# Kernel tuning notes

Hardware: AMD Instinct MI355X
Metric: run time of the kernel (lower is better)

The kernel has to match this reference:

```python
import jax, jax.numpy as jnp
import numpy as np

N_USER = 250_000
N_ITEM = 250_000
E = 500_000
IN, H, C = 128, 64, 2
NEG_SLOPE = 0.01  # torch F.leaky_relu default


def setup_inputs() -> dict:
    key = jax.random.key(0)
    ks = jax.random.split(key, 24)
    d = {}
    d["feat_user"] = jax.random.normal(ks[0], (N_USER, IN), jnp.float32)
    d["feat_item"] = jax.random.normal(ks[1], (N_ITEM, IN), jnp.float32)
    # per-etype linear params, layer 1 (in_feats -> h_dim)
    s1 = 1.0 / np.sqrt(IN)
    d["W1_follows"] = jax.random.normal(ks[2], (IN, H), jnp.float32) * s1
    d["b1_follows"] = jax.random.normal(ks[3], (H,), jnp.float32) * s1
    d["W1_clicks"]  = jax.random.normal(ks[4], (IN, H), jnp.float32) * s1
    d["b1_clicks"]  = jax.random.normal(ks[5], (H,), jnp.float32) * s1
    d["W1_rev"]     = jax.random.normal(ks[6], (IN, H), jnp.float32) * s1
    d["b1_rev"]     = jax.random.normal(ks[7], (H,), jnp.float32) * s1
    # per-etype linear params, layer 2 (h_dim -> num_classes)
    s2 = 1.0 / np.sqrt(H)
    d["W2_follows"] = jax.random.normal(ks[8], (H, C), jnp.float32) * s2
    d["b2_follows"] = jax.random.normal(ks[9], (C,), jnp.float32) * s2
    d["W2_clicks"]  = jax.random.normal(ks[10], (H, C), jnp.float32) * s2
    d["b2_clicks"]  = jax.random.normal(ks[11], (C,), jnp.float32) * s2
    d["W2_rev"]     = jax.random.normal(ks[12], (H, C), jnp.float32) * s2
    d["b2_rev"]     = jax.random.normal(ks[13], (C,), jnp.float32) * s2
    # edge lists: (src, dst) per canonical etype
    d["follows_src"] = jax.random.randint(ks[14], (E,), 0, N_USER, jnp.int32)  # user->user
    d["follows_dst"] = jax.random.randint(ks[15], (E,), 0, N_USER, jnp.int32)
    d["clicks_src"]  = jax.random.randint(ks[16], (E,), 0, N_USER, jnp.int32)  # user->item
    d["clicks_dst"]  = jax.random.randint(ks[17], (E,), 0, N_ITEM, jnp.int32)
    d["rev_src"]     = jax.random.randint(ks[18], (E,), 0, N_ITEM, jnp.int32)  # item->user
    d["rev_dst"]     = jax.random.randint(ks[19], (E,), 0, N_USER, jnp.int32)
    return d


def _mean_agg(Wh, src, dst, n_dst):
    # copy_u + mean: gather transformed src feats per edge, segment-mean onto dst
    m = Wh[src]                                                   # [E, d]
    s = jax.ops.segment_sum(m, dst, num_segments=n_dst)           # [n_dst, d]
    deg = jax.ops.segment_sum(jnp.ones_like(dst, Wh.dtype), dst, num_segments=n_dst)
    return s / jnp.maximum(deg, 1.0)[:, None]                     # 0 for deg-0 nodes (DGL fills 0)


def _layer(fu, fi, Wf, bf, Wc, bc, Wr, br,
           fsrc, fdst, csrc, cdst, rsrc, rdst):
    # per-etype linear on src features, per-etype mean, cross-etype 'sum'
    h_user = (_mean_agg(fu @ Wf + bf, fsrc, fdst, N_USER)
              + _mean_agg(fi @ Wr + br, rsrc, rdst, N_USER))
    h_item = _mean_agg(fu @ Wc + bc, csrc, cdst, N_ITEM)
    return h_user, h_item


def reference(feat_user, feat_item,
              W1_follows, b1_follows, W1_clicks, b1_clicks, W1_rev, b1_rev,
              W2_follows, b2_follows, W2_clicks, b2_clicks, W2_rev, b2_rev,
              follows_src, follows_dst, clicks_src, clicks_dst, rev_src, rev_dst):
    h1u, h1i = _layer(feat_user, feat_item,
                      W1_follows, b1_follows, W1_clicks, b1_clicks, W1_rev, b1_rev,
                      follows_src, follows_dst, clicks_src, clicks_dst, rev_src, rev_dst)
    h2u = jnp.where(h1u >= 0, h1u, NEG_SLOPE * h1u)
    h2i = jnp.where(h1i >= 0, h1i, NEG_SLOPE * h1i)
    out_u, out_i = _layer(h2u, h2i,
                          W2_follows, b2_follows, W2_clicks, b2_clicks, W2_rev, b2_rev,
                          follows_src, follows_dst, clicks_src, clicks_dst, rev_src, rev_dst)
    # (h_dict, h_dict_2) flattened per ntype
    return (out_u, out_i, h2u, h2i)
```

## Files before the change

kernel.cpp:

```cpp
#include <hip/hip_runtime.h>
#include <cstdio>

#define NU 250000
#define NI 250000
#define NE 500000
#define ND 250000
#define NB_SCAN 245
#define NR 8
#define RSZ 31250

typedef __attribute__((ext_vector_type(8))) short short8v;
typedef __attribute__((ext_vector_type(4))) float float4v;

__device__ inline unsigned short f2bf(float x) {
  unsigned int b = __float_as_uint(x);
  unsigned int r = (b + 0x7FFFu + ((b >> 16) & 1u)) >> 16;
  return (unsigned short)r;
}
__device__ inline float bf2f(unsigned short u) {
  return __uint_as_float(((unsigned int)u) << 16);
}

__device__ inline void async_copy16(const float* g, float* l) {
  __builtin_amdgcn_global_load_lds((const __attribute__((address_space(1))) void*)g,
                                   (__attribute__((address_space(3))) void*)l, 16, 0, 0);
}

__global__ void hist3_kernel(const int* __restrict__ fdst, const int* __restrict__ cdst,
                             const int* __restrict__ rdst,
                             int* __restrict__ degf, int* __restrict__ degc, int* __restrict__ degr) {
  int i = blockIdx.x * blockDim.x + threadIdx.x;
  if (i < NE) {
    atomicAdd(&degf[fdst[i]], 1);
    atomicAdd(&degc[cdst[i]], 1);
    atomicAdd(&degr[rdst[i]], 1);
  }
}

__global__ void scan1_kernel(const int* __restrict__ deg0, const int* __restrict__ deg1,
                             const int* __restrict__ deg2, int* __restrict__ bsum) {
  const int* deg = blockIdx.y == 0 ? deg0 : (blockIdx.y == 1 ? deg1 : deg2);
  int* bs = bsum + blockIdx.y * 256;
  __shared__ int s[256];
  int b = blockIdx.x, t = threadIdx.x;
  int base = b * 1024 + t * 4;
  int v = 0;
  #pragma unroll
  for (int i = 0; i < 4; ++i) if (base + i < ND) v += deg[base + i];
  s[t] = v; __syncthreads();
  for (int off = 128; off > 0; off >>= 1) { if (t < off) s[t] += s[t + off]; __syncthreads(); }
  if (t == 0) bs[b] = s[0];
}

__global__ void scan2_kernel(int* __restrict__ bsum) {
  int* bs = bsum + blockIdx.x * 256;
  __shared__ int s[256];
  int t = threadIdx.x;
  s[t] = (t < NB_SCAN) ? bs[t] : 0;
  __syncthreads();
  for (int off = 1; off < 256; off <<= 1) {
    int x = (t >= off) ? s[t - off] : 0;
    __syncthreads();
    s[t] += x;
    __syncthreads();
  }
  if (t < NB_SCAN) bs[t] = (t == 0) ? 0 : s[t - 1];
}

__global__ void scan3_kernel(const int* __restrict__ deg0, const int* __restrict__ deg1,
                             const int* __restrict__ deg2, const int* __restrict__ bsum,
                             int* __restrict__ offs0, int* __restrict__ offs1, int* __restrict__ offs2,
                             int* __restrict__ cur0, int* __restrict__ cur1, int* __restrict__ cur2) {
  int y = blockIdx.y;
  const int* deg = y == 0 ? deg0 : (y == 1 ? deg1 : deg2);
  int* offs = y == 0 ? offs0 : (y == 1 ? offs1 : offs2);
  int* cursor = y == 0 ? cur0 : (y == 1 ? cur1 : cur2);
  const int* bs = bsum + y * 256;
  __shared__ int s[256];
  int b = blockIdx.x, t = threadIdx.x;
  int base = b * 1024 + t * 4;
  int v[4]; int sum = 0;
  #pragma unroll
  for (int i = 0; i < 4; ++i) { v[i] = (base + i < ND) ? deg[base + i] : 0; sum += v[i]; }
  s[t] = sum; __syncthreads();
  for (int off = 1; off < 256; off <<= 1) {
    int x = (t >= off) ? s[t - off] : 0;
    __syncthreads();
    s[t] += x;
    __syncthreads();
  }
  int run = bs[b] + s[t] - sum;
  #pragma unroll
  for (int i = 0; i < 4; ++i) {
    if (base + i < ND) { offs[base + i] = run; cursor[base + i] = run; run += v[i]; }
  }
  if (b == 0 && t == 0) offs[ND] = NE;
}

__global__ void bucket_part_kernel(const int* __restrict__ fsrc, const int* __restrict__ fdst,
                                   const int* __restrict__ csrc, const int* __restrict__ cdst,
                                   const int* __restrict__ rsrc, const int* __restrict__ rdst,
                                   int* __restrict__ curf, int* __restrict__ curc, int* __restrict__ curr,
                                   int* __restrict__ srtf, int* __restrict__ srtc, int* __restrict__ srtr) {
  const int r = blockIdx.x & (NR - 1);
  const int chunk = blockIdx.x >> 3;
  const int lo = r * RSZ, hi = lo + RSZ;
  const int base = chunk * 1024;
  #pragma unroll
  for (int i = 0; i < 4; ++i) {
    int e = base + i * 256 + threadIdx.x;
    if (e < NE) {
      int d0 = fdst[e]; int s0 = fsrc[e];
      if (d0 >= lo && d0 < hi) { int p = atomicAdd(&curf[d0], 1); srtf[p] = s0; }
      int d1 = cdst[e]; int s1 = csrc[e];
      if (d1 >= lo && d1 < hi) { int p = atomicAdd(&curc[d1], 1); srtc[p] = s1; }
      int d2 = rdst[e]; int s2 = rsrc[e];
      if (d2 >= lo && d2 < hi) { int p = atomicAdd(&curr[d2], 1); srtr[p] = s2; }
    }
  }
}

__global__ void prepw_kernel(const float* __restrict__ W0, const float* __restrict__ W1,
                             const float* __restrict__ W2, unsigned short* __restrict__ T) {
  int gt = blockIdx.x * 256 + threadIdx.x;
  int et = gt >> 10;
  int g = gt & 1023;
  int gl = g & 63;
  int jm = (g >> 6) & 3;
  int c = g >> 8;
  int kb = c * 32 + (gl >> 4) * 8;
  int col = jm * 16 + (gl & 15);
  const float* W = et == 0 ? W0 : (et == 1 ? W1 : W2);
  short8v u;
  #pragma unroll
  for (int i = 0; i < 8; ++i) u[i] = (short)f2bf(W[(kb + i) * 64 + col]);
  ((short8v*)T)[gt] = u;
}

template <bool TWO>
__global__ __launch_bounds__(256, 2) void gemm_dma_kernel(
    const float* __restrict__ X, int n, int ntiles,
    const unsigned short* __restrict__ Ta, const float* __restrict__ ba,
    const unsigned short* __restrict__ Tb, const float* __restrict__ bb,
    unsigned short* __restrict__ Ya, unsigned short* __restrict__ Yb) {
  __shared__ float sx[2][64 * 128];
  const int tid = threadIdx.x;
  const int lane = tid & 63;
  const int wave = tid >> 6;
  const int cb = (lane >> 4) * 4;

  short8v A[4][4], B[4][4];
  #pragma unroll
  for (int c = 0; c < 4; ++c) {
    #pragma unroll
    for (int jm = 0; jm < 4; ++jm) {
      A[c][jm] = ((const short8v*)Ta)[c * 256 + jm * 64 + lane];
      if constexpr (TWO) B[c][jm] = ((const short8v*)Tb)[c * 256 + jm * 64 + lane];
    }
  }
  float4 bias_a[4], bias_b[4];
  #pragma unroll
  for (int jm = 0; jm < 4; ++jm) {
    bias_a[jm] = *(const float4*)&ba[jm * 16 + cb];
    if constexpr (TWO) bias_b[jm] = *(const float4*)&bb[jm * 16 + cb];
  }

  const int nl = wave * 16 + (lane & 15);
  const int sw = nl & 7;

  int t = blockIdx.x;
  {
    #pragma unroll
    for (int j = 0; j < 8; ++j) {
      int idx = (wave * 8 + j) * 64 + lane;
      int row = idx >> 5, u = idx & 31;
      int gr = t * 64 + row; if (gr >= n) gr = n - 1;
      const float* src = X + (size_t)gr * 128 + ((u ^ (row & 7)) << 2);
      float* dst = &sx[0][(wave * 8 + j) * 256];
      async_copy16(src, dst);
    }
  }
  asm volatile("s_waitcnt vmcnt(0)" ::: "memory");
  __syncthreads();

  int cur = 0;
  while (true) {
    int tn = t + (int)gridDim.x;
    bool more = (tn < ntiles);
    if (more) {
      #pragma unroll
      for (int j = 0; j < 8; ++j) {
        int idx = (wave * 8 + j) * 64 + lane;
        int row = idx >> 5, u = idx & 31;
        int gr = tn * 64 + row; if (gr >= n) gr = n - 1;
        const float* src = X + (size_t)gr * 128 + ((u ^ (row & 7)) << 2);
        float* dst = &sx[cur ^ 1][(wave * 8 + j) * 256];
        async_copy16(src, dst);
      }
    }

    float4v accA[4] = {};
    float4v accB[4] = {};
    #pragma unroll
    for (int c = 0; c < 4; ++c) {
      int s0 = c * 8 + (lane >> 4) * 2;
      float4 f0 = *(const float4*)&sx[cur][nl * 128 + (((s0 + 0) ^ sw) << 2)];
      float4 f1 = *(const float4*)&sx[cur][nl * 128 + (((s0 + 1) ^ sw) << 2)];
      short8v bfr;
      bfr[0] = (short)f2bf(f0.x); bfr[1] = (short)f2bf(f0.y);
      bfr[2] = (short)f2bf(f0.z); bfr[3] = (short)f2bf(f0.w);
      bfr[4] = (short)f2bf(f1.x); bfr[5] = (short)f2bf(f1.y);
      bfr[6] = (short)f2bf(f1.z); bfr[7] = (short)f2bf(f1.w);
      #pragma unroll
      for (int jm = 0; jm < 4; ++jm) {
        accA[jm] = __builtin_amdgcn_mfma_f32_16x16x32_bf16(A[c][jm], bfr, accA[jm], 0, 0, 0);
        if constexpr (TWO)
          accB[jm] = __builtin_amdgcn_mfma_f32_16x16x32_bf16(B[c][jm], bfr, accB[jm], 0, 0, 0);
      }
    }
    int node = t * 64 + nl;
    if (node < n) {
      #pragma unroll
      for (int jm = 0; jm < 4; ++jm) {
        ushort4 o;
        o.x = f2bf(accA[jm][0] + bias_a[jm].x);
        o.y = f2bf(accA[jm][1] + bias_a[jm].y);
        o.z = f2bf(accA[jm][2] + bias_a[jm].z);
        o.w = f2bf(accA[jm][3] + bias_a[jm].w);
        *(ushort4*)&Ya[(size_t)node * 64 + jm * 16 + cb] = o;
        if constexpr (TWO) {
          ushort4 o2;
          o2.x = f2bf(accB[jm][0] + bias_b[jm].x);
          o2.y = f2bf(accB[jm][1] + bias_b[jm].y);
          o2.z = f2bf(accB[jm][2] + bias_b[jm].z);
          o2.w = f2bf(accB[jm][3] + bias_b[jm].w);
          *(ushort4*)&Yb[(size_t)node * 64 + jm * 16 + cb] = o2;
        }
      }
    }

    if (!more) break;
    asm volatile("s_waitcnt vmcnt(0)" ::: "memory");
    __syncthreads();
    cur ^= 1;
    t = tn;
  }
}

__global__ __launch_bounds__(256) void agg_fused_kernel(
    const unsigned short* __restrict__ Whf, const unsigned short* __restrict__ Whr,
    const unsigned short* __restrict__ Whc,
    const int* __restrict__ offs_f, const int* __restrict__ srt_f,
    const int* __restrict__ offs_r, const int* __restrict__ srt_r,
    const int* __restrict__ offs_c, const int* __restrict__ srt_c,
    const float* __restrict__ W2f, const float* __restrict__ b2f,
    const float* __restrict__ W2c, const float* __restrict__ b2c,
    const float* __restrict__ W2r, const float* __restrict__ b2r,
    float* __restrict__ h2u, float* __restrict__ h2i,
    float* __restrict__ Y2f, float* __restrict__ Y2c, float* __restrict__ Y2r,
    int ub) {
  const int tid = threadIdx.x;
  const int gid = tid >> 4;
  const int q = tid & 15;

  if (blockIdx.x < ub) {
    int d0 = (blockIdx.x * 16 + gid) * 2;
    int d1 = d0 + 1;
    bool v0 = d0 < NU, v1 = d1 < NU;
    int ef0 = v0 ? offs_f[d0] : 0, ef0e = v0 ? offs_f[d0 + 1] : 0;
    int ef1 = v1 ? offs_f[d1] : 0, ef1e = v1 ? offs_f[d1 + 1] : 0;
    int er0 = v0 ? offs_r[d0] : 0, er0e = v0 ? offs_r[d0 + 1] : 0;
    int er1 = v1 ? offs_r[d1] : 0, er1e = v1 ? offs_r[d1 + 1] : 0;
    float rf0 = 1.0f / fmaxf((float)(ef0e - ef0), 1.0f);
    float rf1 = 1.0f / fmaxf((float)(ef1e - ef1), 1.0f);
    float rr0 = 1.0f / fmaxf((float)(er0e - er0), 1.0f);
    float rr1 = 1.0f / fmaxf((float)(er1e - er1), 1.0f);

    float af0[4] = {0, 0, 0, 0}, af1[4] = {0, 0, 0, 0};
    float ar0[4] = {0, 0, 0, 0}, ar1[4] = {0, 0, 0, 0};
    while (ef0 < ef0e || ef1 < ef1e || er0 < er0e || er1 < er1e) {
      bool hf0 = ef0 < ef0e, hf1 = ef1 < ef1e, hr0 = er0 < er0e, hr1 = er1 < er1e;
      ushort4 vf0, vf1, vr0, vr1;
      if (hf0) { int s = srt_f[ef0]; vf0 = *(const ushort4*)&Whf[(size_t)s * 64 + q * 4]; }
      if (hf1) { int s = srt_f[ef1]; vf1 = *(const ushort4*)&Whf[(size_t)s * 64 + q * 4]; }
      if (hr0) { int s = srt_r[er0]; vr0 = *(const ushort4*)&Whr[(size_t)s * 64 + q * 4]; }
      if (hr1) { int s = srt_r[er1]; vr1 = *(const ushort4*)&Whr[(size_t)s * 64 + q * 4]; }
      if (hf0) { af0[0] += bf2f(vf0.x); af0[1] += bf2f(vf0.y); af0[2] += bf2f(vf0.z); af0[3] += bf2f(vf0.w); ++ef0; }
      if (hf1) { af1[0] += bf2f(vf1.x); af1[1] += bf2f(vf1.y); af1[2] += bf2f(vf1.z); af1[3] += bf2f(vf1.w); ++ef1; }
      if (hr0) { ar0[0] += bf2f(vr0.x); ar0[1] += bf2f(vr0.y); ar0[2] += bf2f(vr0.z); ar0[3] += bf2f(vr0.w); ++er0; }
      if (hr1) { ar1[0] += bf2f(vr1.x); ar1[1] += bf2f(vr1.y); ar1[2] += bf2f(vr1.z); ar1[3] += bf2f(vr1.w); ++er1; }
    }

    float h0v[4], h1v[4];
    #pragma unroll
    for (int i = 0; i < 4; ++i) {
      float x0 = af0[i] * rf0 + ar0[i] * rr0;
      h0v[i] = x0 >= 0.f ? x0 : 0.01f * x0;
      float x1 = af1[i] * rf1 + ar1[i] * rr1;
      h1v[i] = x1 >= 0.f ? x1 : 0.01f * x1;
    }
    if (v0) *(float4*)&h2u[(size_t)d0 * 64 + q * 4] = make_float4(h0v[0], h0v[1], h0v[2], h0v[3]);
    if (v1) *(float4*)&h2u[(size_t)d1 * 64 + q * 4] = make_float4(h1v[0], h1v[1], h1v[2], h1v[3]);

    float pf00 = 0, pf01 = 0, pc00 = 0, pc01 = 0;
    float pf10 = 0, pf11 = 0, pc10 = 0, pc11 = 0;
    #pragma unroll
    for (int i = 0; i < 4; ++i) {
      int j = q * 4 + i;
      float wf0 = W2f[j * 2 + 0], wf1 = W2f[j * 2 + 1];
      float wc0 = W2c[j * 2 + 0], wc1 = W2c[j * 2 + 1];
      pf00 += h0v[i] * wf0; pf01 += h0v[i] * wf1;
      pc00 += h0v[i] * wc0; pc01 += h0v[i] * wc1;
      pf10 += h1v[i] * wf0; pf11 += h1v[i] * wf1;
      pc10 += h1v[i] * wc0; pc11 += h1v[i] * wc1;
    }
    #pragma unroll
    for (int off = 1; off < 16; off <<= 1) {
      pf00 += __shfl_xor(pf00, off, 64); pf01 += __shfl_xor(pf01, off, 64);
      pc00 += __shfl_xor(pc00, off, 64); pc01 += __shfl_xor(pc01, off, 64);
      pf10 += __shfl_xor(pf10, off, 64); pf11 += __shfl_xor(pf11, off, 64);
      pc10 += __shfl_xor(pc10, off, 64); pc11 += __shfl_xor(pc11, off, 64);
    }
    if (q == 0) {
      if (v0) {
        Y2f[(size_t)d0 * 2 + 0] = pf00 + b2f[0]; Y2f[(size_t)d0 * 2 + 1] = pf01 + b2f[1];
        Y2c[(size_t)d0 * 2 + 0] = pc00 + b2c[0]; Y2c[(size_t)d0 * 2 + 1] = pc01 + b2c[1];
      }
      if (v1) {
        Y2f[(size_t)d1 * 2 + 0] = pf10 + b2f[0]; Y2f[(size_t)d1 * 2 + 1] = pf11 + b2f[1];
        Y2c[(size_t)d1 * 2 + 0] = pc10 + b2c[0]; Y2c[(size_t)d1 * 2 + 1] = pc11 + b2c[1];
      }
    }
  } else {
    int d0 = ((blockIdx.x - ub) * 16 + gid) * 2;
    int d1 = d0 + 1;
    bool v0 = d0 < NI, v1 = d1 < NI;
    int ec0 = v0 ? offs_c[d0] : 0, ec0e = v0 ? offs_c[d0 + 1] : 0;
    int ec1 = v1 ? offs_c[d1] : 0, ec1e = v1 ? offs_c[d1 + 1] : 0;
    float rc0 = 1.0f / fmaxf((float)(ec0e - ec0), 1.0f);
    float rc1 = 1.0f / fmaxf((float)(ec1e - ec1), 1.0f);

    float ac0[4] = {0, 0, 0, 0}, ac1[4] = {0, 0, 0, 0};
    while (ec0 < ec0e || ec1 < ec1e) {
      bool h0 = ec0 < ec0e, h1 = ec1 < ec1e;
      ushort4 v0v, v1v;
      if (h0) { int s = srt_c[ec0]; v0v = *(const ushort4*)&Whc[(size_t)s * 64 + q * 4]; }
      if (h1) { int s = srt_c[ec1]; v1v = *(const ushort4*)&Whc[(size_t)s * 64 + q * 4]; }
      if (h0) { ac0[0] += bf2f(v0v.x); ac0[1] += bf2f(v0v.y); ac0[2] += bf2f(v0v.z); ac0[3] += bf2f(v0v.w); ++ec0; }
      if (h1) { ac1[0] += bf2f(v1v.x); ac1[1] += bf2f(v1v.y); ac1[2] += bf2f(v1v.z); ac1[3] += bf2f(v1v.w); ++ec1; }
    }

    float h0v[4], h1v[4];
    #pragma unroll
    for (int i = 0; i < 4; ++i) {
      float x0 = ac0[i] * rc0;
      h0v[i] = x0 >= 0.f ? x0 : 0.01f * x0;
      float x1 = ac1[i] * rc1;
      h1v[i] = x1 >= 0.f ? x1 : 0.01f * x1;
    }
    if (v0) *(float4*)&h2i[(size_t)d0 * 64 + q * 4] = make_float4(h0v[0], h0v[1], h0v[2], h0v[3]);
    if (v1) *(float4*)&h2i[(size_t)d1 * 64 + q * 4] = make_float4(h1v[0], h1v[1], h1v[2], h1v[3]);

    float p00 = 0, p01 = 0, p10 = 0, p11 = 0;
    #pragma unroll
    for (int i = 0; i < 4; ++i) {
      int j = q * 4 + i;
      float w0 = W2r[j * 2 + 0], w1 = W2r[j * 2 + 1];
      p00 += h0v[i] * w0; p01 += h0v[i] * w1;
      p10 += h1v[i] * w0; p11 += h1v[i] * w1;
    }
    #pragma unroll
    for (int off = 1; off < 16; off <<= 1) {
      p00 += __shfl_xor(p00, off, 64); p01 += __shfl_xor(p01, off, 64);
      p10 += __shfl_xor(p10, off, 64); p11 += __shfl_xor(p11, off, 64);
    }
    if (q == 0) {
      if (v0) { Y2r[(size_t)d0 * 2 + 0] = p00 + b2r[0]; Y2r[(size_t)d0 * 2 + 1] = p01 + b2r[1]; }
      if (v1) { Y2r[(size_t)d1 * 2 + 0] = p10 + b2r[0]; Y2r[(size_t)d1 * 2 + 1] = p11 + b2r[1]; }
    }
  }
}

__global__ void out_fused_kernel(const float* __restrict__ Y2f, const float* __restrict__ Y2r,
                                 const float* __restrict__ Y2c,
                                 const int* __restrict__ offs_f, const int* __restrict__ srt_f,
                                 const int* __restrict__ offs_r, const int* __restrict__ srt_r,
                                 const int* __restrict__ offs_c, const int* __restrict__ srt_c,
                                 float* __restrict__ out_u, float* __restrict__ out_i, int ub) {
  if (blockIdx.x < ub) {
    int d = blockIdx.x * 256 + threadIdx.x;
    if (d >= NU) return;
    int f = offs_f[d], f1 = offs_f[d + 1];
    int r = offs_r[d], r1 = offs_r[d + 1];
    float rf = 1.0f / fmaxf((float)(f1 - f), 1.0f);
    float rr = 1.0f / fmaxf((float)(r1 - r), 1.0f);
    float a0 = 0.f, a1 = 0.f, c0 = 0.f, c1 = 0.f;
    while (f < f1 || r < r1) {
      bool hf = f < f1, hr = r < r1;
      float2 yf, yr;
      if (hf) { int s = srt_f[f]; yf = *(const float2*)&Y2f[(size_t)s * 2]; }
      if (hr) { int s = srt_r[r]; yr = *(const float2*)&Y2r[(size_t)s * 2]; }
      if (hf) { a0 += yf.x; a1 += yf.y; ++f; }
      if (hr) { c0 += yr.x; c1 += yr.y; ++r; }
    }
    out_u[(size_t)d * 2 + 0] = a0 * rf + c0 * rr;
    out_u[(size_t)d * 2 + 1] = a1 * rf + c1 * rr;
  } else {
    int d = (blockIdx.x - ub) * 256 + threadIdx.x;
    if (d >= NI) return;
    int c = offs_c[d], c1e = offs_c[d + 1];
    float rc = 1.0f / fmaxf((float)(c1e - c), 1.0f);
    float a0 = 0.f, a1 = 0.f;
    for (; c < c1e; ++c) {
      int s = srt_c[c];
      a0 += Y2c[(size_t)s * 2 + 0]; a1 += Y2c[(size_t)s * 2 + 1];
    }
    out_i[(size_t)d * 2 + 0] = a0 * rc;
    out_i[(size_t)d * 2 + 1] = a1 * rc;
  }
}

extern "C" void kernel_launch(void* const* d_in, const int* in_sizes, int n_in,
                              void* d_out, int out_size, void* d_ws, size_t ws_size,
                              hipStream_t stream) {
  const float* feat_user = (const float*)d_in[0];
  const float* feat_item = (const float*)d_in[1];
  const float* W1f = (const float*)d_in[2];  const float* b1f = (const float*)d_in[3];
  const float* W1c = (const float*)d_in[4];  const float* b1c = (const float*)d_in[5];
  const float* W1r = (const float*)d_in[6];  const float* b1r = (const float*)d_in[7];
  const float* W2f = (const float*)d_in[8];  const float* b2f = (const float*)d_in[9];
  const float* W2c = (const float*)d_in[10]; const float* b2c = (const float*)d_in[11];
  const float* W2r = (const float*)d_in[12]; const float* b2r = (const float*)d_in[13];
  const int* fsrc = (const int*)d_in[14];  const int* fdst = (const int*)d_in[15];
  const int* csrc = (const int*)d_in[16];  const int* cdst = (const int*)d_in[17];
  const int* rsrc = (const int*)d_in[18];  const int* rdst = (const int*)d_in[19];

  float* out = (float*)d_out;
  float* out_u = out;
  float* out_i = out + 2 * NU;
  float* h2u  = out + 1000000;
  float* h2i  = out + 17000000;

  unsigned short* Whf = (unsigned short*)d_ws;
  unsigned short* Whc = Whf + 16000000;
  unsigned short* Whr = Whc + 16000000;
  unsigned short* Wtab = Whr + 16000000;
  unsigned short* Tf = Wtab;
  unsigned short* Tc = Wtab + 8192;
  unsigned short* Tr = Wtab + 16384;
  int* ibase = (int*)(Wtab + 24576);
  const int P = 250304;
  int* offs_f = ibase;            int* offs_c = offs_f + P;  int* offs_r = offs_c + P;
  int* cur_f  = offs_r + P;       int* cur_c  = cur_f + P;   int* cur_r  = cur_c + P;
  int* deg_f  = cur_r + P;        int* deg_c  = deg_f + P;   int* deg_r  = deg_c + P;
  int* srt_f  = deg_r + P;
  int* srt_c  = srt_f + 500096;
  int* srt_r  = srt_c + 500096;
  int* bsum   = srt_r + 500096;
  float* Y2f  = (float*)(bsum + 768);
  float* Y2c  = Y2f + 500000;
  float* Y2r  = Y2c + 500000;

  size_t need = 96000000ull + 24576ull * 2ull
              + (9ull * P + 3ull * 500096ull + 768ull + 1500000ull) * 4ull;
  if (ws_size < need) {
    fprintf(stderr, "kernel_launch: ws too small (%zu < %zu)\n", ws_size, need);
    return;
  }

  hipMemsetAsync(deg_f, 0, (size_t)(3 * P) * 4, stream);

  const int eb = (NE + 255) / 256;

  prepw_kernel<<<12, 256, 0, stream>>>(W1f, W1c, W1r, Wtab);

  const int utiles = (NU + 63) / 64;
  const int itiles = (NI + 63) / 64;
  gemm_dma_kernel<true><<<512, 256, 0, stream>>>(feat_user, NU, utiles, Tf, b1f, Tc, b1c, Whf, Whc);
  gemm_dma_kernel<false><<<512, 256, 0, stream>>>(feat_item, NI, itiles, Tr, b1r, nullptr, nullptr, Whr, nullptr);

  hist3_kernel<<<eb, 256, 0, stream>>>(fdst, cdst, rdst, deg_f, deg_c, deg_r);
  scan1_kernel<<<dim3(NB_SCAN, 3), 256, 0, stream>>>(deg_f, deg_c, deg_r, bsum);
  scan2_kernel<<<3, 256, 0, stream>>>(bsum);
  scan3_kernel<<<dim3(NB_SCAN, 3), 256, 0, stream>>>(deg_f, deg_c, deg_r, bsum,
                                                     offs_f, offs_c, offs_r,
                                                     cur_f, cur_c, cur_r);
  const int chunks = (NE + 1023) / 1024;
  bucket_part_kernel<<<chunks * NR, 256, 0, stream>>>(fsrc, fdst, csrc, cdst, rsrc, rdst,
                                                      cur_f, cur_c, cur_r, srt_f, srt_c, srt_r);

  const int ub = (NU + 31) / 32;
  agg_fused_kernel<<<2 * ub, 256, 0, stream>>>(Whf, Whr, Whc,
                                               offs_f, srt_f, offs_r, srt_r, offs_c, srt_c,
                                               W2f, b2f, W2c, b2c, W2r, b2r,
                                               h2u, h2i, Y2f, Y2c, Y2r, ub);

  const int ob = (NU + 255) / 256;
  out_fused_kernel<<<2 * ob, 256, 0, stream>>>(Y2f, Y2r, Y2c,
                                               offs_f, srt_f, offs_r, srt_r, offs_c, srt_c,
                                               out_u, out_i, ob);
}
```

Before: 344.7 us.

## Merge GEMM launches, fold block-sum scan into scan3, use nontemporal stores

The two layer-1 GEMM launches become one persistent kernel that processes user tiles and then item tiles. The scan2 kernel is removed, and each scan3 block rescans the 245 block sums in shared memory itself. Output and intermediate stores switch to nontemporal stores to limit cache pollution. This cuts two launches and their gaps, at the cost of redundant scan work in every scan3 block and possibly worse L2 reuse for Y2 and h2, which later kernels read back.

```diff
diff --git a/kernel.cpp b/kernel.cpp
--- a/kernel.cpp
+++ b/kernel.cpp
@@ -24,6 +24,11 @@
 __device__ inline void async_copy16(const float* g, float* l) {
   __builtin_amdgcn_global_load_lds((const __attribute__((address_space(1))) void*)g,
                                    (__attribute__((address_space(3))) void*)l, 16, 0, 0);
+}
+
+__device__ inline void nt_store4(float* p, float a, float b, float c, float d) {
+  float4v v; v.x = a; v.y = b; v.z = c; v.w = d;
+  __builtin_nontemporal_store(v, (float4v*)p);
 }
 
 __global__ void hist3_kernel(const int* __restrict__ fdst, const int* __restrict__ cdst,
@@ -50,21 +55,6 @@
   s[t] = v; __syncthreads();
   for (int off = 128; off > 0; off >>= 1) { if (t < off) s[t] += s[t + off]; __syncthreads(); }
   if (t == 0) bs[b] = s[0];
-}
-
-__global__ void scan2_kernel(int* __restrict__ bsum) {
-  int* bs = bsum + blockIdx.x * 256;
-  __shared__ int s[256];
-  int t = threadIdx.x;
-  s[t] = (t < NB_SCAN) ? bs[t] : 0;
-  __syncthreads();
-  for (int off = 1; off < 256; off <<= 1) {
-    int x = (t >= off) ? s[t - off] : 0;
-    __syncthreads();
-    s[t] += x;
-    __syncthreads();
-  }
-  if (t < NB_SCAN) bs[t] = (t == 0) ? 0 : s[t - 1];
 }
 
 __global__ void scan3_kernel(const int* __restrict__ deg0, const int* __restrict__ deg1,
@@ -76,8 +66,20 @@
   int* offs = y == 0 ? offs0 : (y == 1 ? offs1 : offs2);
   int* cursor = y == 0 ? cur0 : (y == 1 ? cur1 : cur2);
   const int* bs = bsum + y * 256;
+  __shared__ int sb[256];
   __shared__ int s[256];
   int b = blockIdx.x, t = threadIdx.x;
+
+  sb[t] = (t < NB_SCAN) ? bs[t] : 0;
+  __syncthreads();
+  for (int off = 1; off < 256; off <<= 1) {
+    int x = (t >= off) ? sb[t - off] : 0;
+    __syncthreads();
+    sb[t] += x;
+    __syncthreads();
+  }
+  int blockbase = (b == 0) ? 0 : sb[b - 1];
+
   int base = b * 1024 + t * 4;
   int v[4]; int sum = 0;
   #pragma unroll
@@ -89,7 +91,7 @@
     s[t] += x;
     __syncthreads();
   }
-  int run = bs[b] + s[t] - sum;
+  int run = blockbase + s[t] - sum;
   #pragma unroll
   for (int i = 0; i < 4; ++i) {
     if (base + i < ND) { offs[base + i] = run; cursor[base + i] = run; run += v[i]; }
@@ -138,12 +140,11 @@
 }
 
 template <bool TWO>
-__global__ __launch_bounds__(256, 2) void gemm_dma_kernel(
-    const float* __restrict__ X, int n, int ntiles,
-    const unsigned short* __restrict__ Ta, const float* __restrict__ ba,
-    const unsigned short* __restrict__ Tb, const float* __restrict__ bb,
-    unsigned short* __restrict__ Ya, unsigned short* __restrict__ Yb) {
-  __shared__ float sx[2][64 * 128];
+__device__ inline void gemm_persist(float (*sx)[64 * 128],
+                                    const float* __restrict__ X, int n, int ntiles,
+                                    const unsigned short* __restrict__ Ta, const float* __restrict__ ba,
+                                    const unsigned short* __restrict__ Tb, const float* __restrict__ bb,
+                                    unsigned short* __restrict__ Ya, unsigned short* __restrict__ Yb) {
   const int tid = threadIdx.x;
   const int lane = tid & 63;
   const int wave = tid >> 6;
@@ -169,6 +170,7 @@
   const int sw = nl & 7;
 
   int t = blockIdx.x;
+  if (t >= ntiles) return;
   {
     #pragma unroll
     for (int j = 0; j < 8; ++j) {
@@ -247,6 +249,20 @@
   }
 }
 
+__global__ __launch_bounds__(256, 2) void gemm_both_kernel(
+    const float* __restrict__ Xu, int un, int utiles,
+    const float* __restrict__ Xi, int in_, int itiles,
+    const unsigned short* __restrict__ Tf, const float* __restrict__ b1f,
+    const unsigned short* __restrict__ Tc, const float* __restrict__ b1c,
+    const unsigned short* __restrict__ Tr, const float* __restrict__ b1r,
+    unsigned short* __restrict__ Whf, unsigned short* __restrict__ Whc,
+    unsigned short* __restrict__ Whr) {
+  __shared__ float sx[2][64 * 128];
+  gemm_persist<true>(sx, Xu, un, utiles, Tf, b1f, Tc, b1c, Whf, Whc);
+  __syncthreads();
+  gemm_persist<false>(sx, Xi, in_, itiles, Tr, b1r, nullptr, nullptr, Whr, nullptr);
+}
+
 __global__ __launch_bounds__(256) void agg_fused_kernel(
     const unsigned short* __restrict__ Whf, const unsigned short* __restrict__ Whr,
     const unsigned short* __restrict__ Whc,
@@ -299,8 +315,8 @@
       float x1 = af1[i] * rf1 + ar1[i] * rr1;
       h1v[i] = x1 >= 0.f ? x1 : 0.01f * x1;
     }
-    if (v0) *(float4*)&h2u[(size_t)d0 * 64 + q * 4] = make_float4(h0v[0], h0v[1], h0v[2], h0v[3]);
-    if (v1) *(float4*)&h2u[(size_t)d1 * 64 + q * 4] = make_float4(h1v[0], h1v[1], h1v[2], h1v[3]);
+    if (v0) nt_store4(&h2u[(size_t)d0 * 64 + q * 4], h0v[0], h0v[1], h0v[2], h0v[3]);
+    if (v1) nt_store4(&h2u[(size_t)d1 * 64 + q * 4], h1v[0], h1v[1], h1v[2], h1v[3]);
 
     float pf00 = 0, pf01 = 0, pc00 = 0, pc01 = 0;
     float pf10 = 0, pf11 = 0, pc10 = 0, pc11 = 0;
@@ -323,12 +339,16 @@
     }
     if (q == 0) {
       if (v0) {
-        Y2f[(size_t)d0 * 2 + 0] = pf00 + b2f[0]; Y2f[(size_t)d0 * 2 + 1] = pf01 + b2f[1];
-        Y2c[(size_t)d0 * 2 + 0] = pc00 + b2c[0]; Y2c[(size_t)d0 * 2 + 1] = pc01 + b2c[1];
+        __builtin_nontemporal_store(pf00 + b2f[0], &Y2f[(size_t)d0 * 2 + 0]);
+        __builtin_nontemporal_store(pf01 + b2f[1], &Y2f[(size_t)d0 * 2 + 1]);
+        __builtin_nontemporal_store(pc00 + b2c[0], &Y2c[(size_t)d0 * 2 + 0]);
+        __builtin_nontemporal_store(pc01 + b2c[1], &Y2c[(size_t)d0 * 2 + 1]);
       }
       if (v1) {
-        Y2f[(size_t)d1 * 2 + 0] = pf10 + b2f[0]; Y2f[(size_t)d1 * 2 + 1] = pf11 + b2f[1];
-        Y2c[(size_t)d1 * 2 + 0] = pc10 + b2c[0]; Y2c[(size_t)d1 * 2 + 1] = pc11 + b2c[1];
+        __builtin_nontemporal_store(pf10 + b2f[0], &Y2f[(size_t)d1 * 2 + 0]);
+        __builtin_nontemporal_store(pf11 + b2f[1], &Y2f[(size_t)d1 * 2 + 1]);
+        __builtin_nontemporal_store(pc10 + b2c[0], &Y2c[(size_t)d1 * 2 + 0]);
+        __builtin_nontemporal_store(pc11 + b2c[1], &Y2c[(size_t)d1 * 2 + 1]);
       }
     }
   } else {
@@ -358,8 +378,8 @@
       float x1 = ac1[i] * rc1;
       h1v[i] = x1 >= 0.f ? x1 : 0.01f * x1;
     }
-    if (v0) *(float4*)&h2i[(size_t)d0 * 64 + q * 4] = make_float4(h0v[0], h0v[1], h0v[2], h0v[3]);
-    if (v1) *(float4*)&h2i[(size_t)d1 * 64 + q * 4] = make_float4(h1v[0], h1v[1], h1v[2], h1v[3]);
+    if (v0) nt_store4(&h2i[(size_t)d0 * 64 + q * 4], h0v[0], h0v[1], h0v[2], h0v[3]);
+    if (v1) nt_store4(&h2i[(size_t)d1 * 64 + q * 4], h1v[0], h1v[1], h1v[2], h1v[3]);
 
     float p00 = 0, p01 = 0, p10 = 0, p11 = 0;
     #pragma unroll
@@ -375,8 +395,14 @@
       p10 += __shfl_xor(p10, off, 64); p11 += __shfl_xor(p11, off, 64);
     }
     if (q == 0) {
-      if (v0) { Y2r[(size_t)d0 * 2 + 0] = p00 + b2r[0]; Y2r[(size_t)d0 * 2 + 1] = p01 + b2r[1]; }
-      if (v1) { Y2r[(size_t)d1 * 2 + 0] = p10 + b2r[0]; Y2r[(size_t)d1 * 2 + 1] = p11 + b2r[1]; }
+      if (v0) {
+        __builtin_nontemporal_store(p00 + b2r[0], &Y2r[(size_t)d0 * 2 + 0]);
+        __builtin_nontemporal_store(p01 + b2r[1], &Y2r[(size_t)d0 * 2 + 1]);
+      }
+      if (v1) {
+        __builtin_nontemporal_store(p10 + b2r[0], &Y2r[(size_t)d1 * 2 + 0]);
+        __builtin_nontemporal_store(p11 + b2r[1], &Y2r[(size_t)d1 * 2 + 1]);
+      }
     }
   }
 }
@@ -403,8 +429,8 @@
       if (hf) { a0 += yf.x; a1 += yf.y; ++f; }
       if (hr) { c0 += yr.x; c1 += yr.y; ++r; }
     }
-    out_u[(size_t)d * 2 + 0] = a0 * rf + c0 * rr;
-    out_u[(size_t)d * 2 + 1] = a1 * rf + c1 * rr;
+    __builtin_nontemporal_store(a0 * rf + c0 * rr, &out_u[(size_t)d * 2 + 0]);
+    __builtin_nontemporal_store(a1 * rf + c1 * rr, &out_u[(size_t)d * 2 + 1]);
   } else {
     int d = (blockIdx.x - ub) * 256 + threadIdx.x;
     if (d >= NI) return;
@@ -415,8 +441,8 @@
       int s = srt_c[c];
       a0 += Y2c[(size_t)s * 2 + 0]; a1 += Y2c[(size_t)s * 2 + 1];
     }
-    out_i[(size_t)d * 2 + 0] = a0 * rc;
-    out_i[(size_t)d * 2 + 1] = a1 * rc;
+    __builtin_nontemporal_store(a0 * rc, &out_i[(size_t)d * 2 + 0]);
+    __builtin_nontemporal_store(a1 * rc, &out_i[(size_t)d * 2 + 1]);
   }
 }
 
@@ -468,7 +494,7 @@
     return;
   }
 
-  hipMemsetAsync(deg_f, 0, (size_t)(3 * P) * 4, stream);
+  (void)hipMemsetAsync(deg_f, 0, (size_t)(3 * P) * 4, stream);
 
   const int eb = (NE + 255) / 256;
 
@@ -476,12 +502,11 @@
 
   const int utiles = (NU + 63) / 64;
   const int itiles = (NI + 63) / 64;
-  gemm_dma_kernel<true><<<512, 256, 0, stream>>>(feat_user, NU, utiles, Tf, b1f, Tc, b1c, Whf, Whc);
-  gemm_dma_kernel<false><<<512, 256, 0, stream>>>(feat_item, NI, itiles, Tr, b1r, nullptr, nullptr, Whr, nullptr);
+  gemm_both_kernel<<<512, 256, 0, stream>>>(feat_user, NU, utiles, feat_item, NI, itiles,
+                                            Tf, b1f, Tc, b1c, Tr, b1r, Whf, Whc, Whr);
 
   hist3_kernel<<<eb, 256, 0, stream>>>(fdst, cdst, rdst, deg_f, deg_c, deg_r);
   scan1_kernel<<<dim3(NB_SCAN, 3), 256, 0, stream>>>(deg_f, deg_c, deg_r, bsum);
-  scan2_kernel<<<3, 256, 0, stream>>>(bsum);
   scan3_kernel<<<dim3(NB_SCAN, 3), 256, 0, stream>>>(deg_f, deg_c, deg_r, bsum,
                                                      offs_f, offs_c, offs_r,
                                                      cur_f, cur_c, cur_r);
```

After: 324.4 us, median of 2. 1.06x faster.
